# Kernel optimization log

Hardware: AMD Instinct MI355X
Metric: run time of the kernel (lower is better)

## Reference

```python
import jax, jax.numpy as jnp
import numpy as np

DIM = 2048
DIM_HEAD = 128
HEADS = 16
FF_INNER = 4 * DIM  # 8192
ATTN_INNER = DIM_HEAD * HEADS  # 2048
FUSED_DIMS = (ATTN_INNER, DIM_HEAD, DIM_HEAD, FF_INNER * 2)
R = 8
B, N = 2, 2048


def setup_inputs() -> dict:
    key = jax.random.key(0)
    ks = jax.random.split(key, 12)
    s = 0.02
    return {
        "x": jax.random.normal(ks[0], (B, N, DIM), jnp.float32),
        "gamma": jnp.ones((DIM,), jnp.float32),
        "w_fused": jax.random.normal(ks[1], (DIM, sum(FUSED_DIMS)), jnp.float32) * s,
        "w_attn_out": jax.random.normal(ks[2], (ATTN_INNER, DIM), jnp.float32) * s,
        "w_ff_out": jax.random.normal(ks[3], (FF_INNER, DIM), jnp.float32) * s,
        "a_q": jax.random.normal(ks[4], (DIM, R), jnp.float32) * s,
        "b_q": jax.random.normal(ks[5], (R, ATTN_INNER), jnp.float32) * s,
        "a_k": jax.random.normal(ks[6], (DIM, R), jnp.float32) * s,
        "b_k": jax.random.normal(ks[7], (R, DIM_HEAD), jnp.float32) * s,
        "a_v": jax.random.normal(ks[8], (DIM, R), jnp.float32) * s,
        "b_v": jax.random.normal(ks[9], (R, DIM_HEAD), jnp.float32) * s,
        "a_o": jax.random.normal(ks[10], (ATTN_INNER, R), jnp.float32) * s,
        "b_o": jax.random.normal(ks[11], (R, DIM), jnp.float32) * s,
    }


def _rotate_half(t):
    t1, t2 = jnp.split(t, 2, axis=-1)
    return jnp.concatenate((-t2, t1), axis=-1)


def _rope(pos, t):
    return t * jnp.cos(pos) + _rotate_half(t) * jnp.sin(pos)


def reference(x, gamma, w_fused, w_attn_out, w_ff_out,
              a_q, b_q, a_k, b_k, a_v, b_v, a_o, b_o):
    b, n, d = x.shape
    # LayerNorm (beta buffer is zeros)
    mu = jnp.mean(x, -1, keepdims=True)
    var = jnp.var(x, -1, keepdims=True)
    xn = (x - mu) * jax.lax.rsqrt(var + 1e-5) * gamma

    proj = xn @ w_fused
    splits = np.cumsum(FUSED_DIMS)[:-1]
    q, k, v, ff = jnp.split(proj, splits, axis=-1)

    # fused QKV LoRA (scale alpha/r = 1)
    q = q + (xn @ a_q) @ b_q
    k = k + (xn @ a_k) @ b_k
    v = v + (xn @ a_v) @ b_v

    q = q.reshape(b, n, HEADS, DIM_HEAD).transpose(0, 2, 1, 3)  # b h n d
    q = q * (DIM_HEAD ** -0.5)

    # rotary embedding
    inv_freq = 1.0 / (10000.0 ** (jnp.arange(0, DIM_HEAD, 2, dtype=jnp.float32) / DIM_HEAD))
    freqs = jnp.arange(n, dtype=jnp.float32)[:, None] * inv_freq[None, :]  # n, d/2
    pos = jnp.concatenate((freqs, freqs), axis=-1)  # n, d
    q = _rope(pos, q)          # broadcast over b,h
    k = _rope(pos, k)          # b n d (single head, MQA)

    sim = jnp.einsum('bhid,bjd->bhij', q, k)
    causal = jnp.triu(jnp.ones((n, n), dtype=bool), 1)
    sim = jnp.where(causal, -jnp.finfo(sim.dtype).max, sim)
    attn = jax.nn.softmax(sim, axis=-1)
    out = jnp.einsum('bhij,bjd->bhid', attn, v)
    out = out.transpose(0, 2, 1, 3).reshape(b, n, ATTN_INNER)

    attn_out = out @ w_attn_out + (out @ a_o) @ b_o

    x1, gate = jnp.split(ff, 2, axis=-1)
    ff_out = (jax.nn.silu(gate) * x1) @ w_ff_out
    return attn_out + ff_out
```

## Files before the change

### kernel.cpp

```cpp
#include <hip/hip_runtime.h>

typedef unsigned short u16;
typedef __attribute__((ext_vector_type(8))) short s8v;
typedef __attribute__((ext_vector_type(4))) float f32x4;

__device__ __forceinline__ u16 f2bf(float f) {
  unsigned int u = __float_as_uint(f);
  u += ((u >> 16) & 1u) + 0x7FFFu;
  return (u16)(u >> 16);
}
__device__ __forceinline__ float bf2f(u16 h) {
  return __uint_as_float(((unsigned int)h) << 16);
}
__device__ __forceinline__ void gl_lds16(const void* g, void* l) {
  __builtin_amdgcn_global_load_lds(
      (__attribute__((address_space(1))) void*)g,
      (__attribute__((address_space(3))) void*)l, 16, 0, 0);
}
__device__ __forceinline__ f32x4 mfma16(s8v a, s8v b, f32x4 c) {
  return __builtin_amdgcn_mfma_f32_16x16x32_bf16(a, b, c, 0, 0, 0);
}

__global__ void transpose_cvt(const float* __restrict__ in, u16* __restrict__ out,
                              int rows, int cols, int ldo) {
  __shared__ float tile[32][33];
  int c0 = blockIdx.x * 32, r0 = blockIdx.y * 32;
  int tx = threadIdx.x, ty = threadIdx.y;
#pragma unroll
  for (int i = 0; i < 4; i++)
    tile[ty + i * 8][tx] = in[(long)(r0 + ty + i * 8) * cols + c0 + tx];
  __syncthreads();
#pragma unroll
  for (int i = 0; i < 4; i++)
    out[(long)(c0 + ty + i * 8) * ldo + r0 + tx] = f2bf(tile[tx][ty + i * 8]);
}

__global__ void vtrans(const u16* __restrict__ proj, u16* __restrict__ v_t) {
  __shared__ u16 tile[32][33];
  int n0 = blockIdx.x * 32, d0 = blockIdx.y * 32, b = blockIdx.z;
  int tx = threadIdx.x, ty = threadIdx.y;
#pragma unroll
  for (int i = 0; i < 4; i++)
    tile[ty + i * 8][tx] =
        proj[((long)b * 2048 + n0 + ty + i * 8) * 18688 + 2176 + d0 + tx];
  __syncthreads();
#pragma unroll
  for (int i = 0; i < 4; i++)
    v_t[((long)b * 128 + d0 + ty + i * 8) * 2048 + n0 + tx] = tile[tx][ty + i * 8];
}

__global__ void fill_aug_k(u16* __restrict__ wt, int N, int ldo, int naug,
                           const float* __restrict__ bq, const float* __restrict__ bk,
                           const float* __restrict__ bv) {
  long idx = (long)blockIdx.x * 256 + threadIdx.x;
  if (idx >= (long)N * naug) return;
  int n = (int)(idx / naug), j = (int)(idx % naug);
  float v = 0.f;
  if (bq && j < 8 && n < 2048) v = bq[j * 2048 + n];
  else if (bk && j >= 8 && j < 16 && n >= 2048 && n < 2176) v = bk[(j - 8) * 128 + (n - 2048)];
  else if (bv && j >= 16 && j < 24 && n >= 2176 && n < 2304) v = bv[(j - 16) * 128 + (n - 2176)];
  wt[(long)n * ldo + 2048 + j] = f2bf(v);
}

__global__ __launch_bounds__(256) void layernorm_k(const float* __restrict__ x,
                                                   const float* __restrict__ gamma,
                                                   u16* __restrict__ xn) {
  const int row = blockIdx.x, tid = threadIdx.x;
  const float* xr = x + (long)row * 2048 + tid * 8;
  float4 v0 = *(const float4*)xr;
  float4 v1 = *(const float4*)(xr + 4);
  float vals[8] = {v0.x, v0.y, v0.z, v0.w, v1.x, v1.y, v1.z, v1.w};
  float s = 0.f, q = 0.f;
#pragma unroll
  for (int e = 0; e < 8; e++) { s += vals[e]; q += vals[e] * vals[e]; }
#pragma unroll
  for (int off = 32; off > 0; off >>= 1) {
    s += __shfl_down(s, off, 64);
    q += __shfl_down(q, off, 64);
  }
  __shared__ float red[8];
  const int w = tid >> 6, lane = tid & 63;
  if (lane == 0) { red[w] = s; red[4 + w] = q; }
  __syncthreads();
  if (tid == 0) {
    float S = red[0] + red[1] + red[2] + red[3];
    float Q = red[4] + red[5] + red[6] + red[7];
    float mu = S * (1.f / 2048.f);
    float var = Q * (1.f / 2048.f) - mu * mu;
    red[0] = mu; red[1] = rsqrtf(var + 1e-5f);
  }
  __syncthreads();
  float mu = red[0], rs = red[1];
  const float* g = gamma + tid * 8;
  u16 ov[8];
#pragma unroll
  for (int e = 0; e < 8; e++) ov[e] = f2bf((vals[e] - mu) * rs * g[e]);
  *(s8v*)(xn + (long)row * 2112 + tid * 8) = *(const s8v*)ov;
}

__global__ __launch_bounds__(256) void lora_down_x(u16* __restrict__ xn_aug,
                                                   const float* __restrict__ aq,
                                                   const float* __restrict__ ak,
                                                   const float* __restrict__ av) {
  const int row = blockIdx.x, tid = threadIdx.x;
  s8v xv = *(const s8v*)(xn_aug + (long)row * 2112 + tid * 8);
  float acc[3][8];
#pragma unroll
  for (int m = 0; m < 3; m++)
#pragma unroll
    for (int j = 0; j < 8; j++) acc[m][j] = 0.f;
  const float* mats[3] = {aq, ak, av};
#pragma unroll
  for (int e = 0; e < 8; e++) {
    float xe = bf2f((u16)xv[e]);
    int k = tid * 8 + e;
#pragma unroll
    for (int m = 0; m < 3; m++) {
      const float4* ap = (const float4*)(mats[m] + (long)k * 8);
      float4 a0 = ap[0], a1 = ap[1];
      acc[m][0] += xe * a0.x; acc[m][1] += xe * a0.y;
      acc[m][2] += xe * a0.z; acc[m][3] += xe * a0.w;
      acc[m][4] += xe * a1.x; acc[m][5] += xe * a1.y;
      acc[m][6] += xe * a1.z; acc[m][7] += xe * a1.w;
    }
  }
#pragma unroll
  for (int m = 0; m < 3; m++)
#pragma unroll
    for (int j = 0; j < 8; j++)
#pragma unroll
      for (int off = 32; off > 0; off >>= 1)
        acc[m][j] += __shfl_down(acc[m][j], off, 64);
  __shared__ float red[4][24];
  const int w = tid >> 6, lane = tid & 63;
  if (lane == 0)
    for (int m = 0; m < 3; m++)
      for (int j = 0; j < 8; j++) red[w][m * 8 + j] = acc[m][j];
  __syncthreads();
  if (tid < 64) {
    float v = 0.f;
    if (tid < 24) v = red[0][tid] + red[1][tid] + red[2][tid] + red[3][tid];
    xn_aug[(long)row * 2112 + 2048 + tid] = f2bf(v);
  }
}

__global__ __launch_bounds__(256) void lora_down_ctx(u16* __restrict__ ctx_aug,
                                                     const float* __restrict__ ao) {
  const int row = blockIdx.x, tid = threadIdx.x;
  s8v xv = *(const s8v*)(ctx_aug + (long)row * 2080 + tid * 8);
  float acc[8];
#pragma unroll
  for (int j = 0; j < 8; j++) acc[j] = 0.f;
#pragma unroll
  for (int e = 0; e < 8; e++) {
    float xe = bf2f((u16)xv[e]);
    int k = tid * 8 + e;
    const float4* ap = (const float4*)(ao + (long)k * 8);
    float4 a0 = ap[0], a1 = ap[1];
    acc[0] += xe * a0.x; acc[1] += xe * a0.y; acc[2] += xe * a0.z; acc[3] += xe * a0.w;
    acc[4] += xe * a1.x; acc[5] += xe * a1.y; acc[6] += xe * a1.z; acc[7] += xe * a1.w;
  }
#pragma unroll
  for (int j = 0; j < 8; j++)
#pragma unroll
    for (int off = 32; off > 0; off >>= 1)
      acc[j] += __shfl_down(acc[j], off, 64);
  __shared__ float red[4][8];
  const int w = tid >> 6, lane = tid & 63;
  if (lane == 0)
    for (int j = 0; j < 8; j++) red[w][j] = acc[j];
  __syncthreads();
  if (tid < 32) {
    float v = 0.f;
    if (tid < 8) v = red[0][tid] + red[1][tid] + red[2][tid] + red[3][tid];
    ctx_aug[(long)row * 2080 + 2048 + tid] = f2bf(v);
  }
}

__global__ void rope_k(u16* __restrict__ proj) {
  int idx = blockIdx.x * 256 + threadIdx.x;
  int i = idx & 63;
  int u = (idx >> 6) % 17;
  int row = idx / (17 * 64);
  int n = row & 2047;
  float invf = __powf(10000.f, -(float)i * (1.f / 64.f));
  float ang = (float)n * invf;
  float cs = cosf(ang), sn = sinf(ang);
  int cb = (u < 16) ? u * 128 : 2048;
  u16* p = proj + (long)row * 18688 + cb + i;
  float t1 = bf2f(p[0]), t2 = bf2f(p[64]);
  float sc = (u < 16) ? 0.08838834764831845f : 1.f;
  p[0]  = f2bf((t1 * cs - t2 * sn) * sc);
  p[64] = f2bf((t2 * cs + t1 * sn) * sc);
}

__global__ void silu_mul_k(u16* __restrict__ proj) {
  long idx = (long)blockIdx.x * 256 + threadIdx.x;
  int row = (int)(idx >> 10);
  int c8 = (int)(idx & 1023) * 8;
  u16* px = proj + (long)row * 18688 + 2304 + c8;
  const u16* pg = proj + (long)row * 18688 + 10496 + c8;
  s8v xv = *(const s8v*)px;
  s8v gv = *(const s8v*)pg;
  u16 ov[8];
#pragma unroll
  for (int e = 0; e < 8; e++) {
    float x1 = bf2f((u16)xv[e]);
    float g = bf2f((u16)gv[e]);
    ov[e] = f2bf(x1 * g / (1.f + __expf(-g)));
  }
  *(s8v*)px = *(const s8v*)ov;
}

enum { STORE_BF16 = 0, STORE_F32 = 1, ADD_F32 = 2 };
template <int MODE>
__global__ __launch_bounds__(256, 2) void gemm_bt(const u16* __restrict__ A, int lda,
                                                  const u16* __restrict__ Bt, int ldb,
                                                  void* __restrict__ Cv, int ldc, int K,
                                                  int nbx) {
  const int my = blockIdx.x & 31;
  const int mx = blockIdx.y * 8 + (blockIdx.x >> 5);
  if (mx >= nbx) return;
  __shared__ u16 As[128 * 32];
  __shared__ u16 Bs[128 * 32];
  const int tid = threadIdx.x;
  const int w = tid >> 6, lane = tid & 63, quad = lane >> 4, l15 = lane & 15;
  const int wm = (w >> 1) * 64, wn = (w & 1) * 64;
  const long m0 = (long)my * 128;
  const long n0 = (long)mx * 128;

  const int srow = lane >> 2;
  const int scol = (((lane & 3) ^ ((lane >> 3) & 3)) * 8);
  const int cc0 = w * 2, cc1 = cc0 + 1;
  const u16* ga0 = A + (m0 + cc0 * 16 + srow) * lda + scol;
  const u16* ga1 = A + (m0 + cc1 * 16 + srow) * lda + scol;
  const u16* gb0 = Bt + (n0 + cc0 * 16 + srow) * ldb + scol;
  const u16* gb1 = Bt + (n0 + cc1 * 16 + srow) * ldb + scol;
  u16* la0 = As + cc0 * 512;
  u16* la1 = As + cc1 * 512;
  u16* lb0 = Bs + cc0 * 512;
  u16* lb1 = Bs + cc1 * 512;

  const int sseg = (quad ^ ((l15 >> 1) & 3)) * 8;

  f32x4 acc[4][4];
#pragma unroll
  for (int i = 0; i < 4; i++)
#pragma unroll
    for (int j = 0; j < 4; j++) acc[i][j] = {0.f, 0.f, 0.f, 0.f};

  for (int k0 = 0; k0 < K; k0 += 32) {
    gl_lds16(ga0 + k0, la0);
    gl_lds16(ga1 + k0, la1);
    gl_lds16(gb0 + k0, lb0);
    gl_lds16(gb1 + k0, lb1);
    __syncthreads();
    s8v af[4], bf[4];
#pragma unroll
    for (int mi = 0; mi < 4; mi++)
      af[mi] = *(const s8v*)(As + (wm + mi * 16 + l15) * 32 + sseg);
#pragma unroll
    for (int ni = 0; ni < 4; ni++)
      bf[ni] = *(const s8v*)(Bs + (wn + ni * 16 + l15) * 32 + sseg);
#pragma unroll
    for (int mi = 0; mi < 4; mi++)
#pragma unroll
      for (int ni = 0; ni < 4; ni++)
        acc[mi][ni] = mfma16(af[mi], bf[ni], acc[mi][ni]);
    __syncthreads();
  }
#pragma unroll
  for (int mi = 0; mi < 4; mi++)
#pragma unroll
    for (int r = 0; r < 4; r++) {
      long row = m0 + wm + mi * 16 + quad * 4 + r;
#pragma unroll
      for (int ni = 0; ni < 4; ni++) {
        long col = n0 + wn + ni * 16 + l15;
        float v = acc[mi][ni][r];
        if (MODE == STORE_BF16) ((u16*)Cv)[row * ldc + col] = f2bf(v);
        else if (MODE == STORE_F32) ((float*)Cv)[row * ldc + col] = v;
        else ((float*)Cv)[row * ldc + col] += v;
      }
    }
}

__global__ __launch_bounds__(512, 2) void gemm256_bt(const u16* __restrict__ A,
                                                     const u16* __restrict__ Bt,
                                                     u16* __restrict__ C) {
  __shared__ u16 sh[4 * 16384];
  const int cpx = gridDim.x >> 3;
  const int swz = (blockIdx.x & 7) * cpx + (blockIdx.x >> 3);
  const int bm = swz & 15;
  const int bn = swz >> 4;
  const int tid = threadIdx.x;
  const int w = tid >> 6, lane = tid & 63;
  const int quad = lane >> 4, l15 = lane & 15;
  const int wm = w >> 2, wn = w & 3;
  const int rseg = (quad ^ ((l15 >> 1) & 3)) * 8;
  const int aoff = (wm * 128 + l15) * 32 + rseg;
  const int boff = (wn * 64 + l15) * 32 + rseg;
  const int srow = lane >> 2;
  const int sseg = ((lane & 3) ^ ((lane >> 3) & 3)) * 8;
  const u16* aSrc = A + (long)(bm * 256 + w * 16 + srow) * 2112 + sseg;
  const u16* bSrc = Bt + (long)(bn * 256 + w * 16 + srow) * 2112 + sseg;

  f32x4 acc[8][4];
#pragma unroll
  for (int i = 0; i < 8; i++)
#pragma unroll
    for (int j = 0; j < 4; j++) acc[i][j] = {0.f, 0.f, 0.f, 0.f};

#pragma unroll
  for (int t = 0; t < 3; t++) {
    gl_lds16(aSrc + t * 32, sh + t * 16384 + w * 512);
    gl_lds16(bSrc + t * 32, sh + t * 16384 + 8192 + w * 512);
    gl_lds16(aSrc + 128L * 2112 + t * 32, sh + t * 16384 + 4096 + w * 512);
    gl_lds16(bSrc + 128L * 2112 + t * 32, sh + t * 16384 + 8192 + 4096 + w * 512);
  }
  asm volatile("s_waitcnt vmcnt(8)" ::: "memory");
  __builtin_amdgcn_s_barrier();

  s8v bf[4];
  int kcol = 96;

#define STAGE_UNIT(NB, MH)                                                    \
  gl_lds16(aSrc + (MH) * (128L * 2112) + kcol,                                \
           sh + (NB) * 16384 + (MH) * 4096 + w * 512);                        \
  gl_lds16(bSrc + (MH) * (128L * 2112) + kcol,                                \
           sh + (NB) * 16384 + 8192 + (MH) * 4096 + w * 512);

#define PHASE(CUR, MH, DOB, STG, VM)                                          \
  {                                                                           \
    const u16* Ab = sh + (CUR) * 16384 + aoff + (MH) * 2048;                  \
    s8v af0 = *(const s8v*)(Ab);                                              \
    s8v af1 = *(const s8v*)(Ab + 512);                                        \
    s8v af2 = *(const s8v*)(Ab + 1024);                                       \
    s8v af3 = *(const s8v*)(Ab + 1536);                                       \
    if (DOB) {                                                                \
      const u16* Bb = sh + (CUR) * 16384 + 8192 + boff;                       \
      bf[0] = *(const s8v*)(Bb);                                              \
      bf[1] = *(const s8v*)(Bb + 512);                                        \
      bf[2] = *(const s8v*)(Bb + 1024);                                       \
      bf[3] = *(const s8v*)(Bb + 1536);                                       \
    }                                                                         \
    if (STG) { STAGE_UNIT((((CUR) + 3) & 3), MH) }                            \
    __builtin_amdgcn_s_barrier();                                             \
    __builtin_amdgcn_s_setprio(1);                                            \
    _Pragma("unroll") for (int ni = 0; ni < 4; ni++) {                        \
      acc[(MH) * 4 + 0][ni] = mfma16(af0, bf[ni], acc[(MH) * 4 + 0][ni]);     \
      acc[(MH) * 4 + 1][ni] = mfma16(af1, bf[ni], acc[(MH) * 4 + 1][ni]);     \
      acc[(MH) * 4 + 2][ni] = mfma16(af2, bf[ni], acc[(MH) * 4 + 2][ni]);     \
      acc[(MH) * 4 + 3][ni] = mfma16(af3, bf[ni], acc[(MH) * 4 + 3][ni]);     \
    }                                                                         \
    __builtin_amdgcn_s_setprio(0);                                            \
    if ((VM) == 8) asm volatile("s_waitcnt vmcnt(8)" ::: "memory");           \
    if ((VM) == 4) asm volatile("s_waitcnt vmcnt(4)" ::: "memory");           \
    if ((VM) == 0) asm volatile("s_waitcnt vmcnt(0)" ::: "memory");           \
    __builtin_amdgcn_s_barrier();                                             \
  }

#define TILE(CUR, STG, VM)       \
  PHASE(CUR, 0, 1, STG, -1)      \
  PHASE(CUR, 1, 0, STG, VM)      \
  kcol += 32;

  for (int t4 = 0; t4 < 15; t4++) {
    TILE(0, 1, 8)
    TILE(1, 1, 8)
    TILE(2, 1, 8)
    TILE(3, 1, 8)
  }
  TILE(0, 1, 8)
  TILE(1, 1, 8)
  TILE(2, 1, 8)
  TILE(3, 0, 4)
  TILE(0, 0, 0)
  TILE(1, 0, -1)

#undef TILE
#undef PHASE
#undef STAGE_UNIT

  const long m0 = (long)bm * 256 + wm * 128;
  const long n0 = (long)bn * 256 + wn * 64;
#pragma unroll
  for (int mi = 0; mi < 8; mi++)
#pragma unroll
    for (int r = 0; r < 4; r++) {
      long row = m0 + mi * 16 + quad * 4 + r;
#pragma unroll
      for (int ni = 0; ni < 4; ni++) {
        long col = n0 + ni * 16 + l15;
        C[row * 18688 + col] = f2bf(acc[mi][ni][r]);
      }
    }
}

__global__ __launch_bounds__(256) void flash_k(const u16* __restrict__ proj,
                                               const u16* __restrict__ v_t,
                                               u16* __restrict__ ctx) {
  __shared__ u16 Kt[4 * 1024];
  __shared__ u16 Vx[8 * 512];
  __shared__ u16 Pw[4 * 512];
  const int qt = blockIdx.x, h = blockIdx.y, b = blockIdx.z;
  const int tid = threadIdx.x;
  const int w = tid >> 6, lane = tid & 63, quad = lane >> 4, l15 = lane & 15;
  const int qbase = qt * 64 + w * 16;

  s8v qf[4];
  {
    long rowQ = (long)b * 2048 + qbase + l15;
    const u16* qp = proj + rowQ * 18688 + h * 128 + quad * 8;
#pragma unroll
    for (int kk = 0; kk < 4; kk++) qf[kk] = *(const s8v*)(qp + kk * 32);
  }
  f32x4 o[8];
#pragma unroll
  for (int i = 0; i < 8; i++) o[i] = {0.f, 0.f, 0.f, 0.f};
  float m_i[4] = {-1e30f, -1e30f, -1e30f, -1e30f};
  float l_i[4] = {0.f, 0.f, 0.f, 0.f};

  const int srow = lane >> 2;
  const int sseg = ((lane & 3) ^ ((lane >> 3) & 3)) * 8;
  const int rseg = (quad ^ ((l15 >> 1) & 3)) * 8;

  const int nkb = 2 * qt + 2;
  for (int kb = 0; kb < nkb; kb++) {
    const int k0 = kb * 32;
    {
      long rK = (long)b * 2048 + k0;
#pragma unroll
      for (int h2 = 0; h2 < 2; h2++)
        gl_lds16(proj + (rK + h2 * 16 + srow) * 18688 + 2048 + w * 32 + sseg,
                 Kt + w * 1024 + h2 * 512);
#pragma unroll
      for (int h2 = 0; h2 < 2; h2++)
        gl_lds16(v_t + ((long)b * 128 + w * 32 + h2 * 16 + srow) * 2048 + k0 + sseg,
                 Vx + (w * 2 + h2) * 512);
    }
    __syncthreads();
    if (k0 <= qbase + 15) {
      f32x4 s[2];
#pragma unroll
      for (int ni = 0; ni < 2; ni++) {
        f32x4 a = {0.f, 0.f, 0.f, 0.f};
#pragma unroll
        for (int kk = 0; kk < 4; kk++) {
          s8v kf = *(const s8v*)(Kt + kk * 1024 + (ni * 16 + l15) * 32 + rseg);
          a = mfma16(qf[kk], kf, a);
        }
        s[ni] = a;
      }
#pragma unroll
      for (int ni = 0; ni < 2; ni++) {
        int kg = k0 + ni * 16 + l15;
#pragma unroll
        for (int r = 0; r < 4; r++)
          if (kg > qbase + quad * 4 + r) s[ni][r] = -1e30f;
      }
      float al[4];
#pragma unroll
      for (int r = 0; r < 4; r++) {
        float mx = fmaxf(s[0][r], s[1][r]);
#pragma unroll
        for (int off = 8; off > 0; off >>= 1)
          mx = fmaxf(mx, __shfl_xor(mx, off, 16));
        float mn = fmaxf(m_i[r], mx);
        al[r] = __expf(m_i[r] - mn);
        m_i[r] = mn;
      }
#pragma unroll
      for (int ni = 0; ni < 2; ni++)
#pragma unroll
        for (int r = 0; r < 4; r++) s[ni][r] = __expf(s[ni][r] - m_i[r]);
#pragma unroll
      for (int r = 0; r < 4; r++) {
        float rs = s[0][r] + s[1][r];
#pragma unroll
        for (int off = 8; off > 0; off >>= 1)
          rs += __shfl_xor(rs, off, 16);
        l_i[r] = l_i[r] * al[r] + rs;
      }
#pragma unroll
      for (int ni = 0; ni < 2; ni++)
#pragma unroll
        for (int r = 0; r < 4; r++) {
          int p = quad * 4 + r;
          int sg = ni * 2 + (l15 >> 3);
          int sp = sg ^ ((p >> 1) & 3);
          Pw[w * 512 + p * 32 + sp * 8 + (l15 & 7)] = f2bf(s[ni][r]);
        }
      __asm__ volatile("s_waitcnt lgkmcnt(0)" ::: "memory");
#pragma unroll
      for (int nt = 0; nt < 8; nt++)
#pragma unroll
        for (int r = 0; r < 4; r++) o[nt][r] *= al[r];
      s8v pf = *(const s8v*)(Pw + w * 512 + l15 * 32 + rseg);
#pragma unroll
      for (int nt = 0; nt < 8; nt++) {
        s8v vf = *(const s8v*)(Vx + (nt * 16 + l15) * 32 + rseg);
        o[nt] = mfma16(pf, vf, o[nt]);
      }
    }
    __syncthreads();
  }
  float inv[4];
#pragma unroll
  for (int r = 0; r < 4; r++) inv[r] = 1.f / l_i[r];
#pragma unroll
  for (int nt = 0; nt < 8; nt++)
#pragma unroll
    for (int r = 0; r < 4; r++) {
      long row = (long)b * 2048 + qbase + quad * 4 + r;
      ctx[row * 2080 + h * 128 + nt * 16 + l15] = f2bf(o[nt][r] * inv[r]);
    }
}

#define OFF_WF   0L
#define OFF_WO   78938112L
#define OFF_WFF  87457792L
#define OFF_XN   121012224L
#define OFF_PROJ 138313728L
#define WS_NEED  291405824L

extern "C" void kernel_launch(void* const* d_in, const int* in_sizes, int n_in,
                              void* d_out, int out_size, void* d_ws, size_t ws_size,
                              hipStream_t stream) {
  const float* x       = (const float*)d_in[0];
  const float* gamma   = (const float*)d_in[1];
  const float* w_fused = (const float*)d_in[2];
  const float* w_attn  = (const float*)d_in[3];
  const float* w_ff    = (const float*)d_in[4];
  const float* a_q = (const float*)d_in[5];
  const float* b_q = (const float*)d_in[6];
  const float* a_k = (const float*)d_in[7];
  const float* b_k = (const float*)d_in[8];
  const float* a_v = (const float*)d_in[9];
  const float* b_v = (const float*)d_in[10];
  const float* a_o = (const float*)d_in[11];
  const float* b_o = (const float*)d_in[12];
  float* out = (float*)d_out;
  if (ws_size < (size_t)WS_NEED) return;

  char* ws = (char*)d_ws;
  u16* wf_t    = (u16*)(ws + OFF_WF);
  u16* ctx_aug = (u16*)(ws + OFF_WF);
  u16* wo_t    = (u16*)(ws + OFF_WO);
  u16* wff_t   = (u16*)(ws + OFF_WFF);
  u16* xn_aug  = (u16*)(ws + OFF_XN);
  u16* v_t     = (u16*)(ws + OFF_XN);
  u16* proj    = (u16*)(ws + OFF_PROJ);

  dim3 tb(32, 8);
  transpose_cvt<<<dim3(18688 / 32, 2048 / 32), tb, 0, stream>>>(w_fused, wf_t, 2048, 18688, 2112);
  transpose_cvt<<<dim3(2048 / 32, 2048 / 32), tb, 0, stream>>>(w_attn, wo_t, 2048, 2048, 2080);
  transpose_cvt<<<dim3(2048 / 32, 8192 / 32), tb, 0, stream>>>(w_ff, wff_t, 8192, 2048, 8192);
  fill_aug_k<<<(18688 * 64 + 255) / 256, 256, 0, stream>>>(wf_t, 18688, 2112, 64, b_q, b_k, b_v);
  fill_aug_k<<<(2048 * 32 + 255) / 256, 256, 0, stream>>>(wo_t, 2048, 2080, 32, b_o, nullptr, nullptr);

  layernorm_k<<<4096, 256, 0, stream>>>(x, gamma, xn_aug);
  lora_down_x<<<4096, 256, 0, stream>>>(xn_aug, a_q, a_k, a_v);

  gemm256_bt<<<dim3(16 * (18688 / 256)), 512, 0, stream>>>(xn_aug, wf_t, proj);

  rope_k<<<(4096 * 17 * 64) / 256, 256, 0, stream>>>(proj);
  silu_mul_k<<<(4096 * 1024) / 256, 256, 0, stream>>>(proj);
  vtrans<<<dim3(64, 4, 2), tb, 0, stream>>>(proj, v_t);

  flash_k<<<dim3(32, 16, 2), 256, 0, stream>>>(proj, v_t, ctx_aug);
  lora_down_ctx<<<4096, 256, 0, stream>>>(ctx_aug, a_o);

  gemm_bt<STORE_F32><<<dim3(256, 2), 256, 0, stream>>>(
      ctx_aug, 2080, wo_t, 2080, out, 2048, 2080, 16);
  gemm_bt<ADD_F32><<<dim3(256, 2), 256, 0, stream>>>(
      proj + 2304, 18688, wff_t, 8192, out, 2048, 8192, 16);
}
```

Measured before the change: 1.372 ms.

## Replace output GEMMs with 4-stage pipelined 128x256 kernel and vectorize stores

Replaces the simple single-buffered 128x128 output-projection GEMM with a 512-thread 128x256 tile kernel that keeps three tiles in flight through a 4-slot LDS ring and uses fine-grained vmcnt waits. Both GEMMs now swap the MFMA operands, so each lane holds four consecutive columns and writes them as one packed vector, in bf16 for the fused projection and as float4 for the output. The fused-projection GEMM also drops the barrier before the MFMAs and the barrier after the first phase. This aims to overlap loads with compute and reduce scattered scalar stores, but removing barriers depends on the ring slot ordering staying race-free.

```diff
diff --git a/kernel.cpp b/kernel.cpp
--- a/kernel.cpp
+++ b/kernel.cpp
@@ -2,6 +2,7 @@
 
 typedef unsigned short u16;
 typedef __attribute__((ext_vector_type(8))) short s8v;
+typedef __attribute__((ext_vector_type(4))) short s4v;
 typedef __attribute__((ext_vector_type(4))) float f32x4;
 
 __device__ __forceinline__ u16 f2bf(float f) {
@@ -210,79 +211,6 @@
     ov[e] = f2bf(x1 * g / (1.f + __expf(-g)));
   }
   *(s8v*)px = *(const s8v*)ov;
-}
-
-enum { STORE_BF16 = 0, STORE_F32 = 1, ADD_F32 = 2 };
-template <int MODE>
-__global__ __launch_bounds__(256, 2) void gemm_bt(const u16* __restrict__ A, int lda,
-                                                  const u16* __restrict__ Bt, int ldb,
-                                                  void* __restrict__ Cv, int ldc, int K,
-                                                  int nbx) {
-  const int my = blockIdx.x & 31;
-  const int mx = blockIdx.y * 8 + (blockIdx.x >> 5);
-  if (mx >= nbx) return;
-  __shared__ u16 As[128 * 32];
-  __shared__ u16 Bs[128 * 32];
-  const int tid = threadIdx.x;
-  const int w = tid >> 6, lane = tid & 63, quad = lane >> 4, l15 = lane & 15;
-  const int wm = (w >> 1) * 64, wn = (w & 1) * 64;
-  const long m0 = (long)my * 128;
-  const long n0 = (long)mx * 128;
-
-  const int srow = lane >> 2;
-  const int scol = (((lane & 3) ^ ((lane >> 3) & 3)) * 8);
-  const int cc0 = w * 2, cc1 = cc0 + 1;
-  const u16* ga0 = A + (m0 + cc0 * 16 + srow) * lda + scol;
-  const u16* ga1 = A + (m0 + cc1 * 16 + srow) * lda + scol;
-  const u16* gb0 = Bt + (n0 + cc0 * 16 + srow) * ldb + scol;
-  const u16* gb1 = Bt + (n0 + cc1 * 16 + srow) * ldb + scol;
-  u16* la0 = As + cc0 * 512;
-  u16* la1 = As + cc1 * 512;
-  u16* lb0 = Bs + cc0 * 512;
-  u16* lb1 = Bs + cc1 * 512;
-
-  const int sseg = (quad ^ ((l15 >> 1) & 3)) * 8;
-
-  f32x4 acc[4][4];
-#pragma unroll
-  for (int i = 0; i < 4; i++)
-#pragma unroll
-    for (int j = 0; j < 4; j++) acc[i][j] = {0.f, 0.f, 0.f, 0.f};
-
-  for (int k0 = 0; k0 < K; k0 += 32) {
-    gl_lds16(ga0 + k0, la0);
-    gl_lds16(ga1 + k0, la1);
-    gl_lds16(gb0 + k0, lb0);
-    gl_lds16(gb1 + k0, lb1);
-    __syncthreads();
-    s8v af[4], bf[4];
-#pragma unroll
-    for (int mi = 0; mi < 4; mi++)
-      af[mi] = *(const s8v*)(As + (wm + mi * 16 + l15) * 32 + sseg);
-#pragma unroll
-    for (int ni = 0; ni < 4; ni++)
-      bf[ni] = *(const s8v*)(Bs + (wn + ni * 16 + l15) * 32 + sseg);
-#pragma unroll
-    for (int mi = 0; mi < 4; mi++)
-#pragma unroll
-      for (int ni = 0; ni < 4; ni++)
-        acc[mi][ni] = mfma16(af[mi], bf[ni], acc[mi][ni]);
-    __syncthreads();
-  }
-#pragma unroll
-  for (int mi = 0; mi < 4; mi++)
-#pragma unroll
-    for (int r = 0; r < 4; r++) {
-      long row = m0 + wm + mi * 16 + quad * 4 + r;
-#pragma unroll
-      for (int ni = 0; ni < 4; ni++) {
-        long col = n0 + wn + ni * 16 + l15;
-        float v = acc[mi][ni][r];
-        if (MODE == STORE_BF16) ((u16*)Cv)[row * ldc + col] = f2bf(v);
-        else if (MODE == STORE_F32) ((float*)Cv)[row * ldc + col] = v;
-        else ((float*)Cv)[row * ldc + col] += v;
-      }
-    }
 }
 
 __global__ __launch_bounds__(512, 2) void gemm256_bt(const u16* __restrict__ A,
@@ -345,19 +273,18 @@
       bf[3] = *(const s8v*)(Bb + 1536);                                       \
     }                                                                         \
     if (STG) { STAGE_UNIT((((CUR) + 3) & 3), MH) }                            \
-    __builtin_amdgcn_s_barrier();                                             \
     __builtin_amdgcn_s_setprio(1);                                            \
     _Pragma("unroll") for (int ni = 0; ni < 4; ni++) {                        \
-      acc[(MH) * 4 + 0][ni] = mfma16(af0, bf[ni], acc[(MH) * 4 + 0][ni]);     \
-      acc[(MH) * 4 + 1][ni] = mfma16(af1, bf[ni], acc[(MH) * 4 + 1][ni]);     \
-      acc[(MH) * 4 + 2][ni] = mfma16(af2, bf[ni], acc[(MH) * 4 + 2][ni]);     \
-      acc[(MH) * 4 + 3][ni] = mfma16(af3, bf[ni], acc[(MH) * 4 + 3][ni]);     \
+      acc[(MH) * 4 + 0][ni] = mfma16(bf[ni], af0, acc[(MH) * 4 + 0][ni]);     \
+      acc[(MH) * 4 + 1][ni] = mfma16(bf[ni], af1, acc[(MH) * 4 + 1][ni]);     \
+      acc[(MH) * 4 + 2][ni] = mfma16(bf[ni], af2, acc[(MH) * 4 + 2][ni]);     \
+      acc[(MH) * 4 + 3][ni] = mfma16(bf[ni], af3, acc[(MH) * 4 + 3][ni]);     \
     }                                                                         \
     __builtin_amdgcn_s_setprio(0);                                            \
     if ((VM) == 8) asm volatile("s_waitcnt vmcnt(8)" ::: "memory");           \
     if ((VM) == 4) asm volatile("s_waitcnt vmcnt(4)" ::: "memory");           \
     if ((VM) == 0) asm volatile("s_waitcnt vmcnt(0)" ::: "memory");           \
-    __builtin_amdgcn_s_barrier();                                             \
+    if ((VM) != -1) __builtin_amdgcn_s_barrier();                             \
   }
 
 #define TILE(CUR, STG, VM)       \
@@ -385,16 +312,105 @@
   const long m0 = (long)bm * 256 + wm * 128;
   const long n0 = (long)bn * 256 + wn * 64;
 #pragma unroll
-  for (int mi = 0; mi < 8; mi++)
-#pragma unroll
-    for (int r = 0; r < 4; r++) {
-      long row = m0 + mi * 16 + quad * 4 + r;
-#pragma unroll
-      for (int ni = 0; ni < 4; ni++) {
-        long col = n0 + ni * 16 + l15;
-        C[row * 18688 + col] = f2bf(acc[mi][ni][r]);
+  for (int mi = 0; mi < 8; mi++) {
+    long row = m0 + mi * 16 + l15;
+#pragma unroll
+    for (int ni = 0; ni < 4; ni++) {
+      long col = n0 + ni * 16 + quad * 4;
+      s4v pk = {(short)f2bf(acc[mi][ni][0]), (short)f2bf(acc[mi][ni][1]),
+                (short)f2bf(acc[mi][ni][2]), (short)f2bf(acc[mi][ni][3])};
+      *(s4v*)(C + row * 18688 + col) = pk;
+    }
+  }
+}
+
+enum { STORE_F32 = 1, ADD_F32 = 2 };
+template <int MODE>
+__global__ __launch_bounds__(512, 1) void gemm_out(const u16* __restrict__ A, int lda,
+                                                   const u16* __restrict__ Bt, int ldb,
+                                                   float* __restrict__ Cv, int ldc, int K) {
+  __shared__ u16 sh[4 * 12288];
+  const int cpx = gridDim.x >> 3;
+  const int swz = (blockIdx.x & 7) * cpx + (blockIdx.x >> 3);
+  const int bm = swz & 31;
+  const int bn = swz >> 5;
+  const int tid = threadIdx.x;
+  const int w = tid >> 6, lane = tid & 63;
+  const int quad = lane >> 4, l15 = lane & 15;
+  const int wm = w >> 2, wn = w & 3;
+  const int rseg = (quad ^ ((l15 >> 1) & 3)) * 8;
+  const int aoff = (wm * 64 + l15) * 32 + rseg;
+  const int boff = 4096 + (wn * 64 + l15) * 32 + rseg;
+  const int srow = lane >> 2;
+  const int sseg = ((lane & 3) ^ ((lane >> 3) & 3)) * 8;
+  const u16* aSrc = A + (long)(bm * 128 + w * 16 + srow) * lda + sseg;
+  const u16* bSrc0 = Bt + (long)(bn * 256 + w * 16 + srow) * ldb + sseg;
+  const u16* bSrc1 = Bt + (long)(bn * 256 + 128 + w * 16 + srow) * ldb + sseg;
+  const int NT = K >> 5;
+
+  f32x4 acc[4][4];
+#pragma unroll
+  for (int i = 0; i < 4; i++)
+#pragma unroll
+    for (int j = 0; j < 4; j++) acc[i][j] = {0.f, 0.f, 0.f, 0.f};
+
+#pragma unroll
+  for (int t = 0; t < 3; t++) {
+    gl_lds16(aSrc + t * 32, sh + t * 12288 + w * 512);
+    gl_lds16(bSrc0 + t * 32, sh + t * 12288 + 4096 + w * 512);
+    gl_lds16(bSrc1 + t * 32, sh + t * 12288 + 8192 + w * 512);
+  }
+  asm volatile("s_waitcnt vmcnt(6)" ::: "memory");
+  __builtin_amdgcn_s_barrier();
+
+  int kcol = 96;
+  for (int t = 0; t < NT; ++t) {
+    const int cur = (t & 3) * 12288;
+    const u16* Ab = sh + cur + aoff;
+    const u16* Bb = sh + cur + boff;
+    s8v af[4], bf[4];
+#pragma unroll
+    for (int mi = 0; mi < 4; mi++) af[mi] = *(const s8v*)(Ab + mi * 512);
+#pragma unroll
+    for (int ni = 0; ni < 4; ni++) bf[ni] = *(const s8v*)(Bb + ni * 512);
+    if (t < NT - 3) {
+      const int nb = ((t + 3) & 3) * 12288;
+      gl_lds16(aSrc + kcol, sh + nb + w * 512);
+      gl_lds16(bSrc0 + kcol, sh + nb + 4096 + w * 512);
+      gl_lds16(bSrc1 + kcol, sh + nb + 8192 + w * 512);
+      kcol += 32;
+    }
+    __builtin_amdgcn_s_setprio(1);
+#pragma unroll
+    for (int mi = 0; mi < 4; mi++)
+#pragma unroll
+      for (int ni = 0; ni < 4; ni++)
+        acc[mi][ni] = mfma16(bf[ni], af[mi], acc[mi][ni]);
+    __builtin_amdgcn_s_setprio(0);
+    if (t < NT - 3)       asm volatile("s_waitcnt vmcnt(6)" ::: "memory");
+    else if (t == NT - 3) asm volatile("s_waitcnt vmcnt(3)" ::: "memory");
+    else if (t == NT - 2) asm volatile("s_waitcnt vmcnt(0)" ::: "memory");
+    if (t != NT - 1) __builtin_amdgcn_s_barrier();
+  }
+
+  const long m0 = (long)bm * 128 + wm * 64;
+  const long n0 = (long)bn * 256 + wn * 64;
+#pragma unroll
+  for (int mi = 0; mi < 4; mi++) {
+    long row = m0 + mi * 16 + l15;
+#pragma unroll
+    for (int ni = 0; ni < 4; ni++) {
+      long col = n0 + ni * 16 + quad * 4;
+      float* p = Cv + row * ldc + col;
+      if (MODE == STORE_F32) {
+        *(f32x4*)p = acc[mi][ni];
+      } else {
+        f32x4 old = *(const f32x4*)p;
+        old += acc[mi][ni];
+        *(f32x4*)p = old;
       }
     }
+  }
 }
 
 __global__ __launch_bounds__(256) void flash_k(const u16* __restrict__ proj,
@@ -571,8 +587,8 @@
   flash_k<<<dim3(32, 16, 2), 256, 0, stream>>>(proj, v_t, ctx_aug);
   lora_down_ctx<<<4096, 256, 0, stream>>>(ctx_aug, a_o);
 
-  gemm_bt<STORE_F32><<<dim3(256, 2), 256, 0, stream>>>(
-      ctx_aug, 2080, wo_t, 2080, out, 2048, 2080, 16);
-  gemm_bt<ADD_F32><<<dim3(256, 2), 256, 0, stream>>>(
-      proj + 2304, 18688, wff_t, 8192, out, 2048, 8192, 16);
-}
+  gemm_out<STORE_F32><<<dim3(256), 512, 0, stream>>>(
+      ctx_aug, 2080, wo_t, 2080, out, 2048, 2080);
+  gemm_out<ADD_F32><<<dim3(256), 512, 0, stream>>>(
+      proj + 2304, 18688, wff_t, 8192, out, 2048, 8192);
+}
```

New measurement: 1.315 ms. 4.2% less time.
